# Optimization experiments

Hardware: AMD Instinct MI355X
Metric: run time of the kernel (lower is better)

Reference implementation:

```python
import jax, jax.numpy as jnp
import numpy as np

B, S, D = 2, 2048, 2048
H, KVH = 32, 8
HD = D // H          # 64
N_REP = H // KVH     # 4
NEG = -1e9


def setup_inputs() -> dict:
    key = jax.random.key(0)
    ks = jax.random.split(key, 5)
    x = jax.random.normal(ks[0], (B, S, D), dtype=jnp.float32)
    std = 0.02
    wq = jax.random.normal(ks[1], (H * HD, D), dtype=jnp.float32) * std
    wk = jax.random.normal(ks[2], (KVH * HD, D), dtype=jnp.float32) * std
    wv = jax.random.normal(ks[3], (KVH * HD, D), dtype=jnp.float32) * std
    wo = jax.random.normal(ks[4], (D, H * HD), dtype=jnp.float32) * std
    # RoPE tables: (S, HD//2)
    inv_freq = 1.0 / (10000.0 ** (np.arange(0, HD, 2, dtype=np.float32) / HD))
    t = np.arange(S, dtype=np.float32)
    freqs = np.outer(t, inv_freq)
    freqs_cos = jnp.asarray(np.cos(freqs))
    freqs_sin = jnp.asarray(np.sin(freqs))
    # additive causal mask [1,1,S,S]
    causal = np.tril(np.ones((S, S), dtype=bool))
    mask = jnp.asarray(np.where(causal, 0.0, NEG).astype(np.float32))[None, None]
    return {"x": x, "wq": wq, "wk": wk, "wv": wv, "wo": wo,
            "freqs_cos": freqs_cos, "freqs_sin": freqs_sin, "mask": mask}


def _apply_rope(t, cos, sin):
    # t: [B,S,nh,HD]; cos/sin: [S, HD//2]
    tr = t.reshape(t.shape[:-1] + (HD // 2, 2))
    r, i = tr[..., 0], tr[..., 1]
    c = cos[None, :, None, :]
    s = sin[None, :, None, :]
    out_r = r * c - i * s
    out_i = r * s + i * c
    return jnp.stack([out_r, out_i], axis=-1).reshape(t.shape)


def reference(x, wq, wk, wv, wo, freqs_cos, freqs_sin, mask):
    b, s, _ = x.shape
    q = (x @ wq.T).reshape(b, s, H, HD)
    k = (x @ wk.T).reshape(b, s, KVH, HD)
    v = (x @ wv.T).reshape(b, s, KVH, HD)
    q = _apply_rope(q, freqs_cos, freqs_sin)
    k = _apply_rope(k, freqs_cos, freqs_sin)
    # repeat_kv (GQA expansion) then move heads forward: [B,H,S,HD]
    k = jnp.repeat(k, N_REP, axis=2)
    v = jnp.repeat(v, N_REP, axis=2)
    q = q.transpose(0, 2, 1, 3)
    k = k.transpose(0, 2, 1, 3)
    v = v.transpose(0, 2, 1, 3)
    scale = 1.0 / jnp.sqrt(jnp.float32(HD))
    scores = jnp.einsum("bhqd,bhkd->bhqk", q, k) * scale + mask[:, :, :s, :s]
    attn = jax.nn.softmax(scores, axis=-1)
    out = jnp.einsum("bhqk,bhkd->bhqd", attn, v)
    out = out.transpose(0, 2, 1, 3).reshape(b, s, H * HD)
    return out @ wo.T
```

## Files before the change

kernel.cpp:

```cpp
#include <hip/hip_runtime.h>
#include <hip/hip_bf16.h>
#include <stdint.h>


#define NEG_BIG (-1e9f)
#define SCALE_LOG2 0.18033688011112042f
#define DEFER_THR 10.0f

typedef __bf16 bf16x8 __attribute__((ext_vector_type(8)));
typedef float f32x4 __attribute__((ext_vector_type(4)));
typedef float f32x16 __attribute__((ext_vector_type(16)));
typedef uint16_t u16x8 __attribute__((ext_vector_type(8)));
typedef uint32_t u32x4 __attribute__((ext_vector_type(4)));

__device__ inline uint16_t f2bf(float x) {
    __hip_bfloat16 h = __float2bfloat16(x);
    return __builtin_bit_cast(uint16_t, h);
}
__device__ inline float bf2f(uint16_t u) {
    uint32_t t = (uint32_t)u << 16;
    return __builtin_bit_cast(float, t);
}

__device__ inline void async_cp16(const void* g, void* l) {
    __builtin_amdgcn_global_load_lds(
        (const __attribute__((address_space(1))) uint32_t*)g,
        (__attribute__((address_space(3))) uint32_t*)l,
        16 , 0 , 0 );
}

__global__ void cvt4(const float* __restrict__ in, uint16_t* __restrict__ out, int n4) {
    int i = blockIdx.x * blockDim.x + threadIdx.x;
    if (i >= n4) return;
    const float4 v = ((const float4*)in)[i];
    ushort4 o;
    o.x = f2bf(v.x); o.y = f2bf(v.y); o.z = f2bf(v.z); o.w = f2bf(v.w);
    ((ushort4*)out)[i] = o;
}

__global__ void build_wqkv(const float* __restrict__ wq, const float* __restrict__ wk,
                           const float* __restrict__ wv, uint16_t* __restrict__ out) {
    int i = blockIdx.x * blockDim.x + threadIdx.x;
    if (i >= (3072 * 2048) / 4) return;
    int e = i * 4;
    int row = e >> 11;
    int col = e & 2047;
    const float* src = (row < 2048) ? (wq + (long)row * 2048 + col)
                     : (row < 2560) ? (wk + (long)(row - 2048) * 2048 + col)
                                    : (wv + (long)(row - 2560) * 2048 + col);
    const float4 v = *(const float4*)src;
    ushort4 o;
    o.x = f2bf(v.x); o.y = f2bf(v.y); o.z = f2bf(v.z); o.w = f2bf(v.w);
    ((ushort4*)(out + e))[0] = o;
}

template <int BN, int OUT_BF16>
__global__ __launch_bounds__(512) void gemm256(const uint16_t* __restrict__ A,
                                               const uint16_t* __restrict__ Bw,
                                               void* __restrict__ Cout,
                                               int M, int N, int K) {
    constexpr int WN = BN / 4;
    constexpr int NF = WN / 16;
    constexpr int BROUNDS = BN / 64;

    __shared__ __align__(16) uint16_t As[2][256 * 64];
    __shared__ __align__(16) uint16_t Bs[2][BN * 64];

    const int tid = threadIdx.x;
    const int l = tid & 63;
    const int w = tid >> 6;
    const int wmi = w >> 2;
    const int wni = w & 3;
    const int c = l & 15, g = l >> 4;
    const long row0 = (long)blockIdx.x * 256;
    const long col0 = (long)blockIdx.y * BN;

    f32x4 acc[8][NF] = {};

    auto STAGE = [&](int buf, int t) {
        const long k0 = (long)t * 64;
#pragma unroll
        for (int rr = 0; rr < 4; ++rr) {
            const int e = rr * 512 + tid;
            const int r = e >> 3;
            const int gs = (e & 7) ^ (r & 7);
            async_cp16(A + (row0 + r) * (long)K + k0 + gs * 8, &As[buf][e * 8]);
        }
#pragma unroll
        for (int rr = 0; rr < BROUNDS; ++rr) {
            const int e = rr * 512 + tid;
            const int r = e >> 3;
            const int gs = (e & 7) ^ (r & 7);
            async_cp16(Bw + (col0 + r) * (long)K + k0 + gs * 8, &Bs[buf][e * 8]);
        }
    };

    STAGE(0, 0);
    __syncthreads();

    const int nt = K / 64;
    for (int t = 0; t < nt; ++t) {
        const int cur = t & 1;
        if (t + 1 < nt) STAGE(cur ^ 1, t + 1);

#pragma unroll
        for (int kk = 0; kk < 2; ++kk) {
            bf16x8 bF[NF];
#pragma unroll
            for (int n = 0; n < NF; ++n) {
                const int rb = wni * WN + n * 16 + c;
                const int sp = ((kk * 4 + g) ^ (c & 7));
                bF[n] = *(const bf16x8*)&Bs[cur][rb * 64 + sp * 8];
            }
#pragma unroll
            for (int mh = 0; mh < 2; ++mh) {
                bf16x8 aF[4];
#pragma unroll
                for (int mm = 0; mm < 4; ++mm) {
                    const int ra = wmi * 128 + (mh * 4 + mm) * 16 + c;
                    const int sp = ((kk * 4 + g) ^ (c & 7));
                    aF[mm] = *(const bf16x8*)&As[cur][ra * 64 + sp * 8];
                }
                __builtin_amdgcn_s_setprio(1);
#pragma unroll
                for (int mm = 0; mm < 4; ++mm)
#pragma unroll
                    for (int n = 0; n < NF; ++n)
                        acc[mh * 4 + mm][n] = __builtin_amdgcn_mfma_f32_16x16x32_bf16(
                            aF[mm], bF[n], acc[mh * 4 + mm][n], 0, 0, 0);
                __builtin_amdgcn_s_setprio(0);
            }
        }
        if (t + 1 < nt) __syncthreads();
    }

#pragma unroll
    for (int m = 0; m < 8; ++m) {
        const long rg = row0 + wmi * 128 + m * 16 + g * 4;
#pragma unroll
        for (int n = 0; n < NF; ++n) {
            const long cg = col0 + wni * WN + n * 16 + c;
#pragma unroll
            for (int r = 0; r < 4; ++r) {
                float v = acc[m][n][r];
                if (OUT_BF16)
                    ((uint16_t*)Cout)[(rg + r) * (long)N + cg] = f2bf(v);
                else
                    ((float*)Cout)[(rg + r) * (long)N + cg] = v;
            }
        }
    }
}

__global__ void rope_q(uint16_t* __restrict__ qkv,
                       const float* __restrict__ cosT,
                       const float* __restrict__ sinT) {
    int idx = blockIdx.x * blockDim.x + threadIdx.x;
    if (idx >= 4096 * 1024) return;
    int m = idx >> 10;
    int j = idx & 1023;
    int s = m & 2047;
    int d2 = j & 31;
    float cc = cosT[s * 32 + d2];
    float ss = sinT[s * 32 + d2];
    uint32_t* p = (uint32_t*)(qkv + (long)m * 3072 + 2 * j);
    uint32_t v = *p;
    float re = bf2f((uint16_t)(v & 0xffffu));
    float im = bf2f((uint16_t)(v >> 16));
    float orr = (re * cc - im * ss) * SCALE_LOG2;
    float oi  = (re * ss + im * cc) * SCALE_LOG2;
    *p = (uint32_t)f2bf(orr) | ((uint32_t)f2bf(oi) << 16);
}

__global__ void pack_kv(const uint16_t* __restrict__ qkv,
                        const float* __restrict__ cosT,
                        const float* __restrict__ sinT,
                        uint16_t* __restrict__ Kpk,
                        uint16_t* __restrict__ Vpk) {
    const int gw = (blockIdx.x * blockDim.x + threadIdx.x) >> 6;
    const int l = threadIdx.x & 63;
    const int lq = l & 31, hi = l >> 5;
    if (gw < 4096) {
        const int wid = gw;
        const int s = wid & 3;
        const int tile = (wid >> 2) & 63;
        const int bk = wid >> 8;
        const int b = bk >> 3, kvh = bk & 7;
        const int key = 32 * tile + lq;
        const uint16_t* src = qkv + (long)(b * 2048 + key) * 3072
                            + 2048 + kvh * 64 + 16 * s + 8 * hi;
        u16x8 v = *(const u16x8*)src;
        const int d2b = 8 * s + 4 * hi;
        u16x8 o;
#pragma unroll
        for (int p = 0; p < 4; ++p) {
            const float cc = cosT[key * 32 + d2b + p];
            const float ss = sinT[key * 32 + d2b + p];
            const float re = bf2f(v[2 * p]);
            const float im = bf2f(v[2 * p + 1]);
            o[2 * p]     = f2bf(re * cc - im * ss);
            o[2 * p + 1] = f2bf(re * ss + im * cc);
        }
        *(u16x8*)(Kpk + (((long)(bk * 64 + tile) * 4 + s) * 64 + l) * 8) = o;
    } else {
        const int wid = gw - 4096;
        const int s2 = wid & 1;
        const int nd = (wid >> 1) & 1;
        const int tile = (wid >> 2) & 63;
        const int bk = wid >> 8;
        const int b = bk >> 3, kvh = bk & 7;
        const int key0 = 32 * tile + 16 * s2 + 8 * hi;
        const uint16_t* src = qkv + (long)(b * 2048 + key0) * 3072
                            + 2560 + kvh * 64 + nd * 32 + lq;
        u16x8 v;
#pragma unroll
        for (int jj = 0; jj < 8; ++jj) v[jj] = src[(long)jj * 3072];
        *(u16x8*)(Vpk + ((((long)(bk * 64 + tile) * 2 + nd) * 2 + s2) * 64 + l) * 8) = v;
    }
}

__device__ inline void pack_pf(const float pr[16], int hi, bf16x8 pf[2]) {
    uint32_t wds[8], xw[8];
#pragma unroll
    for (int m = 0; m < 8; ++m)
        wds[m] = (uint32_t)f2bf(pr[2 * m]) | ((uint32_t)f2bf(pr[2 * m + 1]) << 16);
#pragma unroll
    for (int m = 0; m < 8; ++m)
        xw[m] = (uint32_t)__shfl_xor((int)wds[m], 32);
#pragma unroll
    for (int s = 0; s < 2; ++s) {
        u32x4 pk;
        pk[0] = hi ? xw[4 * s + 2] : wds[4 * s + 0];
        pk[1] = hi ? xw[4 * s + 3] : wds[4 * s + 1];
        pk[2] = hi ? wds[4 * s + 2] : xw[4 * s + 0];
        pk[3] = hi ? wds[4 * s + 3] : xw[4 * s + 1];
        pf[s] = __builtin_bit_cast(bf16x8, pk);
    }
}

__global__ __launch_bounds__(128) void attn_fwd(const uint16_t* __restrict__ qkv,
                                                const uint16_t* __restrict__ Kpk,
                                                const uint16_t* __restrict__ Vpk,
                                                uint16_t* __restrict__ outb) {
    const int bid = blockIdx.x;
    const int bhp = bid & 31;
    const int j = 63 - (bid >> 5);
    const int t0 = threadIdx.x;
    const int l = t0 & 63, ww = t0 >> 6;
    const int gh = 2 * bhp + ww;
    const int b = gh >> 5, h = gh & 31;
    const int kvh = h >> 2;
    const int bk = b * 8 + kvh;
    const int lq = l & 31, hi = l >> 5;
    const int q = 32 * j + lq;

    const uint16_t* qrow = qkv + (long)(b * 2048 + q) * 3072 + h * 64 + 8 * hi;
    bf16x8 qf[4];
#pragma unroll
    for (int s = 0; s < 4; ++s) qf[s] = *(const bf16x8*)(qrow + 16 * s);

    float m_run = -1e30f, l_run = 0.f;
    f32x16 accO[2] = {};

    const uint16_t* kbase = Kpk + (long)bk * 64 * 2048 + (long)l * 8;
    const uint16_t* vbase = Vpk + (long)bk * 64 * 2048 + (long)l * 8;
    const int nT = (j + 2) >> 1;

    for (int t = 0; t < nT; ++t) {
        bf16x8 kf[2][4];
#pragma unroll
        for (int u = 0; u < 2; ++u)
#pragma unroll
            for (int s = 0; s < 4; ++s)
                kf[u][s] = *(const bf16x8*)(kbase + (long)(2 * t + u) * 2048 + s * 512);

        f32x16 st0 = {}, st1 = {};
        __builtin_amdgcn_s_setprio(1);
#pragma unroll
        for (int s = 0; s < 4; ++s)
            st0 = __builtin_amdgcn_mfma_f32_32x32x16_bf16(kf[0][s], qf[s], st0, 0, 0, 0);
#pragma unroll
        for (int s = 0; s < 4; ++s)
            st1 = __builtin_amdgcn_mfma_f32_32x32x16_bf16(kf[1][s], qf[s], st1, 0, 0, 0);
        __builtin_amdgcn_s_setprio(0);

        bf16x8 vf[2][2][2];
#pragma unroll
        for (int u = 0; u < 2; ++u)
#pragma unroll
            for (int nd = 0; nd < 2; ++nd)
#pragma unroll
                for (int s2 = 0; s2 < 2; ++s2)
                    vf[u][nd][s2] = *(const bf16x8*)(vbase + (long)(2 * t + u) * 2048 + nd * 1024 + s2 * 512);

        if (t == nT - 1) {
            const int tq0 = lq + ((j - 2 * t) << 5) - 4 * hi;
            const int tq1 = tq0 - 32;
#pragma unroll
            for (int r = 0; r < 16; ++r) {
                const int kc = (r & 3) + 8 * (r >> 2);
                if (kc > tq0) st0[r] = NEG_BIG;
                if (kc > tq1) st1[r] = NEG_BIG;
            }
        }

        float mx[16];
#pragma unroll
        for (int r = 0; r < 16; ++r) mx[r] = fmaxf(st0[r], st1[r]);
#pragma unroll
        for (int off = 8; off; off >>= 1)
#pragma unroll
            for (int r = 0; r < 8; ++r)
                if (r < off) mx[r] = fmaxf(mx[r], mx[r + off]);
        const float vm = fmaxf(mx[0], __shfl_xor(mx[0], 32));

        if (!__all(vm - m_run <= DEFER_THR)) {
            const float mnew = fmaxf(m_run, vm);
            const float alpha = __builtin_amdgcn_exp2f(m_run - mnew);
            m_run = mnew;
            l_run *= alpha;
#pragma unroll
            for (int nd = 0; nd < 2; ++nd)
#pragma unroll
                for (int r = 0; r < 16; ++r) accO[nd][r] *= alpha;
        }

        float pr0[16], pr1[16], sm[8];
#pragma unroll
        for (int r = 0; r < 16; ++r) pr0[r] = __builtin_amdgcn_exp2f(st0[r] - m_run);
#pragma unroll
        for (int r = 0; r < 16; ++r) pr1[r] = __builtin_amdgcn_exp2f(st1[r] - m_run);
#pragma unroll
        for (int m = 0; m < 8; ++m)
            sm[m] = (pr0[2 * m] + pr0[2 * m + 1]) + (pr1[2 * m] + pr1[2 * m + 1]);
#pragma unroll
        for (int off = 4; off; off >>= 1)
#pragma unroll
            for (int r = 0; r < 4; ++r)
                if (r < off) sm[r] += sm[r + off];
        l_run += sm[0] + __shfl_xor(sm[0], 32);

        bf16x8 pf0[2], pf1[2];
        pack_pf(pr0, hi, pf0);
        pack_pf(pr1, hi, pf1);

        __builtin_amdgcn_s_setprio(1);
#pragma unroll
        for (int nd = 0; nd < 2; ++nd) {
            accO[nd] = __builtin_amdgcn_mfma_f32_32x32x16_bf16(vf[0][nd][0], pf0[0], accO[nd], 0, 0, 0);
            accO[nd] = __builtin_amdgcn_mfma_f32_32x32x16_bf16(vf[0][nd][1], pf0[1], accO[nd], 0, 0, 0);
            accO[nd] = __builtin_amdgcn_mfma_f32_32x32x16_bf16(vf[1][nd][0], pf1[0], accO[nd], 0, 0, 0);
            accO[nd] = __builtin_amdgcn_mfma_f32_32x32x16_bf16(vf[1][nd][1], pf1[1], accO[nd], 0, 0, 0);
        }
        __builtin_amdgcn_s_setprio(0);
    }

    const float invl = 1.0f / l_run;
    uint16_t* orow = outb + (long)(b * 2048 + q) * 2048 + h * 64 + 4 * hi;
#pragma unroll
    for (int nd = 0; nd < 2; ++nd)
#pragma unroll
        for (int m = 0; m < 4; ++m) {
            ushort4 o;
            o.x = f2bf(accO[nd][4 * m + 0] * invl);
            o.y = f2bf(accO[nd][4 * m + 1] * invl);
            o.z = f2bf(accO[nd][4 * m + 2] * invl);
            o.w = f2bf(accO[nd][4 * m + 3] * invl);
            *(ushort4*)(orow + nd * 32 + 8 * m) = o;
        }
}

extern "C" void kernel_launch(void* const* d_in, const int* in_sizes, int n_in,
                              void* d_out, int out_size, void* d_ws, size_t ws_size,
                              hipStream_t stream) {
    const float* x    = (const float*)d_in[0];
    const float* wq   = (const float*)d_in[1];
    const float* wk   = (const float*)d_in[2];
    const float* wv   = (const float*)d_in[3];
    const float* wo   = (const float*)d_in[4];
    const float* fcos = (const float*)d_in[5];
    const float* fsin = (const float*)d_in[6];
    float* out = (float*)d_out;

    uint8_t* ws = (uint8_t*)d_ws;
    const size_t MiB = 1048576;
    uint16_t* x_bf   = (uint16_t*)(ws);
    uint16_t* w_bf   = (uint16_t*)(ws + 16 * MiB);
    uint16_t* qkv_bf = (uint16_t*)(ws + 28 * MiB);
    uint16_t* att_bf = x_bf;
    uint16_t* Kpk    = (uint16_t*)(ws + 16 * MiB);
    uint16_t* Vpk    = (uint16_t*)(ws + 20 * MiB);
    uint16_t* wo_bf  = (uint16_t*)(ws + 16 * MiB);

    cvt4<<<(2097152 + 255) / 256, 256, 0, stream>>>(x, x_bf, 2097152);
    build_wqkv<<<(1572864 + 255) / 256, 256, 0, stream>>>(wq, wk, wv, w_bf);

    gemm256<192, 1><<<dim3(16, 16), 512, 0, stream>>>(x_bf, w_bf, qkv_bf, 4096, 3072, 2048);

    rope_q<<<16384, 256, 0, stream>>>(qkv_bf, fcos, fsin);
    pack_kv<<<2048, 256, 0, stream>>>(qkv_bf, fcos, fsin, Kpk, Vpk);

    attn_fwd<<<2048, 128, 0, stream>>>(qkv_bf, Kpk, Vpk, att_bf);

    cvt4<<<(1048576 + 255) / 256, 256, 0, stream>>>(wo, wo_bf, 1048576);
    gemm256<128, 0><<<dim3(16, 16), 512, 0, stream>>>(att_bf, wo_bf, out, 4096, 2048, 2048);
}
```

Before: 212.4 us.

## Split attention KV range across two waves with LDS merge, use permlane32 swap

Each block now handles one head and one 32-query tile, with its two waves splitting the key tiles in half and merging partial softmax state (max, sum, accumulator) through shared memory. The grid doubles to 4096 blocks to raise parallelism and shorten the causal critical path. The P-fragment repack replaces shuffles and selects with v_permlane32_swap, and launch bounds request 4 blocks per SIMD-level occupancy hint. The cost is extra LDS traffic, a block barrier, and uneven halves when nT is odd.

```diff
diff --git a/kernel.cpp b/kernel.cpp
--- a/kernel.cpp
+++ b/kernel.cpp
@@ -219,41 +219,39 @@
     }
 }
 
-__device__ inline void pack_pf(const float pr[16], int hi, bf16x8 pf[2]) {
-    uint32_t wds[8], xw[8];
+__device__ inline void pack_pf(const float pr[16], bf16x8 pf[2]) {
+    uint32_t wds[8];
 #pragma unroll
     for (int m = 0; m < 8; ++m)
         wds[m] = (uint32_t)f2bf(pr[2 * m]) | ((uint32_t)f2bf(pr[2 * m + 1]) << 16);
-#pragma unroll
-    for (int m = 0; m < 8; ++m)
-        xw[m] = (uint32_t)__shfl_xor((int)wds[m], 32);
-#pragma unroll
-    for (int s = 0; s < 2; ++s) {
-        u32x4 pk;
-        pk[0] = hi ? xw[4 * s + 2] : wds[4 * s + 0];
-        pk[1] = hi ? xw[4 * s + 3] : wds[4 * s + 1];
-        pk[2] = hi ? wds[4 * s + 2] : xw[4 * s + 0];
-        pk[3] = hi ? wds[4 * s + 3] : xw[4 * s + 1];
-        pf[s] = __builtin_bit_cast(bf16x8, pk);
-    }
-}
-
-__global__ __launch_bounds__(128) void attn_fwd(const uint16_t* __restrict__ qkv,
-                                                const uint16_t* __restrict__ Kpk,
-                                                const uint16_t* __restrict__ Vpk,
-                                                uint16_t* __restrict__ outb) {
+    asm volatile("v_permlane32_swap_b32 %0, %1" : "+v"(wds[0]), "+v"(wds[2]));
+    asm volatile("v_permlane32_swap_b32 %0, %1" : "+v"(wds[1]), "+v"(wds[3]));
+    asm volatile("v_permlane32_swap_b32 %0, %1" : "+v"(wds[4]), "+v"(wds[6]));
+    asm volatile("v_permlane32_swap_b32 %0, %1" : "+v"(wds[5]), "+v"(wds[7]));
+    u32x4 pk0 = {wds[0], wds[1], wds[2], wds[3]};
+    u32x4 pk1 = {wds[4], wds[5], wds[6], wds[7]};
+    pf[0] = __builtin_bit_cast(bf16x8, pk0);
+    pf[1] = __builtin_bit_cast(bf16x8, pk1);
+}
+
+__global__ __launch_bounds__(128, 4) void attn_fwd(const uint16_t* __restrict__ qkv,
+                                                   const uint16_t* __restrict__ Kpk,
+                                                   const uint16_t* __restrict__ Vpk,
+                                                   uint16_t* __restrict__ outb) {
     const int bid = blockIdx.x;
-    const int bhp = bid & 31;
-    const int j = 63 - (bid >> 5);
+    const int gh = bid & 63;
+    const int j = 63 - (bid >> 6);
     const int t0 = threadIdx.x;
     const int l = t0 & 63, ww = t0 >> 6;
-    const int gh = 2 * bhp + ww;
     const int b = gh >> 5, h = gh & 31;
     const int kvh = h >> 2;
     const int bk = b * 8 + kvh;
     const int lq = l & 31, hi = l >> 5;
     const int q = 32 * j + lq;
 
+    __shared__ float smM[64], smL[64];
+    __shared__ float smO[64][33];
+
     const uint16_t* qrow = qkv + (long)(b * 2048 + q) * 3072 + h * 64 + 8 * hi;
     bf16x8 qf[4];
 #pragma unroll
@@ -265,8 +263,11 @@
     const uint16_t* kbase = Kpk + (long)bk * 64 * 2048 + (long)l * 8;
     const uint16_t* vbase = Vpk + (long)bk * 64 * 2048 + (long)l * 8;
     const int nT = (j + 2) >> 1;
-
-    for (int t = 0; t < nT; ++t) {
+    const int h0 = nT >> 1;
+    const int tbeg = ww ? h0 : 0;
+    const int tend = ww ? nT : h0;
+
+    for (int t = tbeg; t < tend; ++t) {
         bf16x8 kf[2][4];
 #pragma unroll
         for (int u = 0; u < 2; ++u)
@@ -341,8 +342,8 @@
         l_run += sm[0] + __shfl_xor(sm[0], 32);
 
         bf16x8 pf0[2], pf1[2];
-        pack_pf(pr0, hi, pf0);
-        pack_pf(pr1, hi, pf1);
+        pack_pf(pr0, pf0);
+        pack_pf(pr1, pf1);
 
         __builtin_amdgcn_s_setprio(1);
 #pragma unroll
@@ -355,19 +356,37 @@
         __builtin_amdgcn_s_setprio(0);
     }
 
-    const float invl = 1.0f / l_run;
-    uint16_t* orow = outb + (long)(b * 2048 + q) * 2048 + h * 64 + 4 * hi;
-#pragma unroll
-    for (int nd = 0; nd < 2; ++nd)
-#pragma unroll
-        for (int m = 0; m < 4; ++m) {
-            ushort4 o;
-            o.x = f2bf(accO[nd][4 * m + 0] * invl);
-            o.y = f2bf(accO[nd][4 * m + 1] * invl);
-            o.z = f2bf(accO[nd][4 * m + 2] * invl);
-            o.w = f2bf(accO[nd][4 * m + 3] * invl);
-            *(ushort4*)(orow + nd * 32 + 8 * m) = o;
-        }
+    if (ww == 0) {
+        smM[l] = m_run;
+        smL[l] = l_run;
+#pragma unroll
+        for (int nd = 0; nd < 2; ++nd)
+#pragma unroll
+            for (int r = 0; r < 16; ++r) smO[l][nd * 16 + r] = accO[nd][r];
+    }
+    __syncthreads();
+    if (ww == 1) {
+        const float m0 = smM[l], l0 = smL[l];
+        const float mf = fmaxf(m0, m_run);
+        const float a0 = __builtin_amdgcn_exp2f(m0 - mf);
+        const float a1 = __builtin_amdgcn_exp2f(m_run - mf);
+        const float lf = l0 * a0 + l_run * a1;
+        const float invl = 1.0f / lf;
+        uint16_t* orow = outb + (long)(b * 2048 + q) * 2048 + h * 64 + 4 * hi;
+#pragma unroll
+        for (int nd = 0; nd < 2; ++nd)
+#pragma unroll
+            for (int m = 0; m < 4; ++m) {
+                ushort4 o;
+#pragma unroll
+                for (int r4 = 0; r4 < 4; ++r4) {
+                    const int r = 4 * m + r4;
+                    const float vmerged = smO[l][nd * 16 + r] * a0 + accO[nd][r] * a1;
+                    ((uint16_t*)&o)[r4] = f2bf(vmerged * invl);
+                }
+                *(ushort4*)(orow + nd * 32 + 8 * m) = o;
+            }
+    }
 }
 
 extern "C" void kernel_launch(void* const* d_in, const int* in_sizes, int n_in,
@@ -400,7 +419,7 @@
     rope_q<<<16384, 256, 0, stream>>>(qkv_bf, fcos, fsin);
     pack_kv<<<2048, 256, 0, stream>>>(qkv_bf, fcos, fsin, Kpk, Vpk);
 
-    attn_fwd<<<2048, 128, 0, stream>>>(qkv_bf, Kpk, Vpk, att_bf);
+    attn_fwd<<<4096, 128, 0, stream>>>(qkv_bf, Kpk, Vpk, att_bf);
 
     cvt4<<<(1048576 + 255) / 256, 256, 0, stream>>>(wo, wo_bf, 1048576);
     gemm256<128, 0><<<dim3(16, 16), 512, 0, stream>>>(att_bf, wo_bf, out, 4096, 2048, 2048);
```

Result: no change. 212.7 us (+0.1%).
